# Kernel tuning notes

Hardware: AMD Instinct MI355X
Metric: run time of the kernel (lower is better)

## Reference

```python
import math
import jax, jax.numpy as jnp
import numpy as np
from jax import lax

UP = 2
DOWN = 2
M = 8
BETA = 2.5
FC = 0.5          # up_fc = down_fc = 0.5 (not 'critical' branch)
LRELU = 0.1

def _lpf_filter(factor):
    # Kaiser-windowed sinc, matches Resampler.__init__ (fc != 'critical' branch)
    Mf = M * factor
    n = np.arange(-Mf // 2, Mf // 2 + 1).astype(np.float32)   # 17 taps
    cutoff = FC * math.pi
    f = np.sin(cutoff * n) / (math.pi * n + 1e-8)
    f[len(n) // 2] = FC
    win = np.kaiser(Mf + 1, BETA).astype(np.float32)          # == torch.kaiser_window(.., periodic=False)
    return jnp.asarray(win * f, dtype=jnp.float32)

UP_FILT = _lpf_filter(UP)
DOWN_FILT = _lpf_filter(DOWN)

def _conv1d_same(x, w, groups=1):
    # x: (B, Cin, L), w: (Cout, Cin//groups, K) with odd K
    pad = (w.shape[-1] - 1) // 2
    return lax.conv_general_dilated(x, w, window_strides=(1,), padding=[(pad, pad)],
                                    dimension_numbers=('NCH', 'OIH', 'NCH'),
                                    feature_group_count=groups)

def _lpf(x, filt):
    # depthwise grouped FIR, padding='same'
    C = x.shape[1]
    f = jnp.broadcast_to(filt[None, None, :], (C, 1, filt.shape[0]))
    return _conv1d_same(x, f, groups=C)

def setup_inputs() -> dict:
    key = jax.random.key(0)
    ks = jax.random.split(key, 4)
    bs, c_in, c_out, w_dim, L, k = 16, 512, 512, 512, 2048, 3
    return {
        'x': jax.random.normal(ks[0], (bs, c_in, L), dtype=jnp.float32),
        'w': jax.random.normal(ks[1], (bs, w_dim), dtype=jnp.float32),
        'affine_w': jax.random.normal(ks[2], (c_in, w_dim), dtype=jnp.float32) * 0.02,
        'affine_b': jnp.ones((c_in,), dtype=jnp.float32),
        'conv_w': jax.random.normal(ks[3], (c_out, c_in, k), dtype=jnp.float32) * 0.05,
        'conv_b': jnp.zeros((c_out,), dtype=jnp.float32),
        'norm_ema': jnp.ones((), dtype=jnp.float32),
    }

def reference(x, w, affine_w, affine_b, conv_w, conv_b, norm_ema):
    # eval mode, equalized_lr=False, normalize=True
    x = x * lax.rsqrt(norm_ema)
    cond = w @ affine_w.T + affine_b                                      # (bs, c_in)
    # weight / style normalization
    Wn = conv_w * lax.rsqrt(jnp.mean(jnp.square(conv_w), axis=(1, 2), keepdims=True))
    s = cond * lax.rsqrt(jnp.mean(jnp.square(cond)))                      # (bs, c_in)
    # demod coeff: rsqrt(sum_{i,k} (Wn[o,i,k]*s[b,i])^2 + 1e-8)
    d = lax.rsqrt(jnp.einsum('oik,bi->bo', jnp.square(Wn), jnp.square(s)) + 1e-8)
    # modulate-conv-demodulate (equivalent to per-sample grouped conv with conv_w[None]*s*d)
    y = _conv1d_same(x * s[:, :, None], Wn) * d[:, :, None] + conv_b[None, :, None]
    # upsample: zero-insertion then interpolation LPF
    bs, C, L = y.shape
    y = jnp.pad(y[..., None], ((0, 0), (0, 0), (0, 0), (0, UP - 1))).reshape(bs, C, L * UP)
    y = _lpf(y, UP_FILT)
    # filtered nonlinearity
    y = jax.nn.leaky_relu(y, LRELU) * math.sqrt(2)
    # downsample: anti-alias LPF then decimate
    y = _lpf(y, DOWN_FILT)[:, :, ::DOWN]
    return y
```

## Files before the change

### kernel.cpp

```cpp
#include <hip/hip_runtime.h>
#include <cmath>

typedef __attribute__((ext_vector_type(8))) short short8;
typedef __attribute__((ext_vector_type(4))) float f32x4;

static __device__ __forceinline__ unsigned short f2bf(float x) {
  unsigned int u = __float_as_uint(x);
  unsigned int r = (u + 0x7FFFu + ((u >> 16) & 1u)) >> 16;
  return (unsigned short)r;
}
static __device__ __forceinline__ float bf2f(unsigned short u) {
  return __uint_as_float(((unsigned int)u) << 16);
}
static __device__ __forceinline__ void glds16(const unsigned short* g, unsigned short* l) {
  __builtin_amdgcn_global_load_lds((const __attribute__((address_space(1))) unsigned int*)(g),
                                   (__attribute__((address_space(3))) unsigned int*)(l), 16, 0, 0);
}

#define VWAIT(n) asm volatile("s_waitcnt vmcnt(" #n ")" ::: "memory")

__global__ __launch_bounds__(256) void k_pre1(const float* __restrict__ w,
    const float* __restrict__ aw, const float* __restrict__ ab,
    const float* __restrict__ cw, float* __restrict__ cond, float* __restrict__ ssum,
    float* __restrict__ W2, float* __restrict__ rinv, unsigned short* __restrict__ wpack) {
  __shared__ float red[4];
  int bid = blockIdx.x, t = threadIdx.x;
  if (bid < 128) {
    int outp = bid * 64 + (t >> 2);
    int sub = t & 3;
    int b = outp >> 9, i = outp & 511;
    const float4* wr = (const float4*)(w + b * 512);
    const float4* ar = (const float4*)(aw + i * 512);
    float acc = 0.f;
    #pragma unroll
    for (int jj = 0; jj < 32; ++jj) {
      int j = sub + jj * 4;
      float4 a = ar[j], v = wr[j];
      acc += a.x * v.x + a.y * v.y + a.z * v.z + a.w * v.w;
    }
    acc += __shfl_xor(acc, 1);
    acc += __shfl_xor(acc, 2);
    float s = 0.f;
    if (sub == 0) {
      float c = acc + ab[i];
      cond[outp] = c;
      s = c * c;
    }
    #pragma unroll
    for (int off = 4; off <= 32; off <<= 1) s += __shfl_xor(s, off);
    if ((t & 63) == 0) atomicAdd(ssum, s);
  } else {
    int o = bid - 128;
    const float* row = cw + o * 1536;
    float local = 0.f;
    for (int r = 0; r < 2; ++r) {
      int i = t + 256 * r;
      float a = row[3 * i], b = row[3 * i + 1], c = row[3 * i + 2];
      float w2 = a * a + b * b + c * c;
      W2[o * 512 + i] = w2;
      local += w2;
      int chunk = i >> 5;
      int laneo = (((i >> 3) & 3) << 4) + (o & 15);
      int e = i & 7;
      int base = (chunk * 32 + (o >> 4)) * 512 + laneo * 8 + e;
      wpack[base] = f2bf(a);
      wpack[base + 16 * 32 * 512] = f2bf(b);
      wpack[base + 2 * 16 * 32 * 512] = f2bf(c);
    }
    #pragma unroll
    for (int off = 32; off >= 1; off >>= 1) local += __shfl_down(local, off);
    if ((t & 63) == 0) red[t >> 6] = local;
    __syncthreads();
    if (t == 0) {
      float m = red[0] + red[1] + red[2] + red[3];
      rinv[o] = rsqrtf(m * (1.f / 1536.f));
    }
  }
}

__global__ __launch_bounds__(256) void k_pre2(const float* __restrict__ x,
    const float* __restrict__ W2, const float* __restrict__ cond,
    const float* __restrict__ rinv, const float* __restrict__ ssum,
    const float* __restrict__ nrm, float* __restrict__ coef,
    unsigned short* __restrict__ xsT) {
  __shared__ float shb[64 * 65];
  int bid = blockIdx.x, t = threadIdx.x;
  if (bid < 256) {
    int og = bid & 15, b = bid >> 4;
    int o = og * 32 + (t >> 3);
    int il = t & 7;
    float c0 = cond[b * 512 + t];
    float c1 = cond[b * 512 + t + 256];
    shb[t] = c0 * c0;
    shb[t + 256] = c1 * c1;
    __syncthreads();
    float acc = 0.f;
    #pragma unroll
    for (int jj = 0; jj < 16; ++jj) {
      int i = jj * 32 + il * 4;
      float4 wv = *(const float4*)(W2 + o * 512 + i);
      acc += wv.x * shb[i] + wv.y * shb[i + 1] + wv.z * shb[i + 2] + wv.w * shb[i + 3];
    }
    acc += __shfl_xor(acc, 1);
    acc += __shfl_xor(acc, 2);
    acc += __shfl_xor(acc, 4);
    if (il == 0) {
      float inv_ms = 8192.f / ssum[0];
      float ro = rinv[o];
      coef[b * 512 + o] = ro * rsqrtf(ro * ro * acc * inv_ms + 1e-8f);
    }
  } else {
    int xb = bid - 256;
    int lb = xb & 31, ib = (xb >> 5) & 7, b = xb >> 8;
    float (*tile)[65] = (float(*)[65])shb;
    int l0 = lb * 64, i0 = ib * 64;
    float sc = rsqrtf(ssum[0] * (1.f / 8192.f)) * rsqrtf(nrm[0]);
    int tr = t >> 4, tc = (t & 15) * 4;
    #pragma unroll
    for (int rr = 0; rr < 4; ++rr) {
      int il = rr * 16 + tr;
      float se = cond[b * 512 + i0 + il] * sc;
      float4 v = *(const float4*)(x + ((size_t)b * 512 + i0 + il) * 2048 + l0 + tc);
      tile[il][tc + 0] = v.x * se;
      tile[il][tc + 1] = v.y * se;
      tile[il][tc + 2] = v.z * se;
      tile[il][tc + 3] = v.w * se;
    }
    __syncthreads();
    int lr = t >> 3, ic = (t & 7) * 8;
    #pragma unroll
    for (int rr = 0; rr < 2; ++rr) {
      int ll = rr * 32 + lr;
      uint4 u;
      unsigned int pk[4];
      #pragma unroll
      for (int j = 0; j < 4; ++j) {
        unsigned short lo = f2bf(tile[ic + 2 * j][ll]);
        unsigned short hi = f2bf(tile[ic + 2 * j + 1][ll]);
        pk[j] = (unsigned int)lo | ((unsigned int)hi << 16);
      }
      u.x = pk[0]; u.y = pk[1]; u.z = pk[2]; u.w = pk[3];
      *(uint4*)(xsT + ((size_t)b * 2050 + 1 + l0 + ll) * 512 + i0 + ic) = u;
    }
    if (lb == 0 && t < 8) {
      uint4 z; z.x = 0; z.y = 0; z.z = 0; z.w = 0;
      *(uint4*)(xsT + ((size_t)b * 2050) * 512 + i0 + t * 8) = z;
    }
    if (lb == 31 && t < 8) {
      uint4 z; z.x = 0; z.y = 0; z.z = 0; z.w = 0;
      *(uint4*)(xsT + ((size_t)b * 2050 + 2049) * 512 + i0 + t * 8) = z;
    }
  }
}

#define STAGE_B(buf, c) { \
  _Pragma("unroll") for (int j_ = 0; j_ < 3; ++j_) { \
    int sb_ = wave * 130 + ((j_ < 2) ? j_ * 64 : 128); \
    int s_ = sb_ + ((j_ < 2) ? lane : (lane & 1)); \
    if (j_ < 2 || lane < 2) { \
      int col_ = ((s_ >> 3) << 1) | (((s_ >> 2) ^ (s_ >> 4)) & 1); \
      int q_ = ((s_ ^ (s_ >> 2) ^ (s_ >> 4)) & 1) | ((((s_ >> 1) ^ (s_ >> 3)) & 1) << 1); \
      const unsigned short* src_ = xsT + ((size_t)b * 2050 + l0 + col_) * 512 + (c) * 32 + q_ * 8; \
      glds16(src_, &Bl[buf][sb_ * 8]); \
    } \
  } }

#define LOAD_A(Ar, c) { \
  _Pragma("unroll") for (int k_ = 0; k_ < 3; ++k_) \
  _Pragma("unroll") for (int rg_ = 0; rg_ < 4; ++rg_) \
    Ar[k_ * 4 + rg_] = *(const short8*)(wpack + ((size_t)((k_ * 16 + (c)) * 32 + ob * 8 + wr * 4 + rg_)) * 512 + lane * 8); }

#define MFMA_STEP(Ar, buf) { \
  _Pragma("unroll") for (int k_ = 0; k_ < 3; ++k_) { \
    short8 bfr_[4]; \
    _Pragma("unroll") for (int cg_ = 0; cg_ < 4; ++cg_) { \
      int col_ = wc * 64 + cg_ * 16 + (lane & 15) + k_; \
      int byte_ = (col_ * 64 + ((lane >> 4) << 4)) ^ ((col_ & 7) << 4); \
      bfr_[cg_] = *(const short8*)((const char*)Bl[buf] + byte_); \
    } \
    _Pragma("unroll") for (int rg_ = 0; rg_ < 4; ++rg_) \
      _Pragma("unroll") for (int cg_ = 0; cg_ < 4; ++cg_) \
        acc[rg_][cg_] = __builtin_amdgcn_mfma_f32_16x16x32_bf16(Ar[k_ * 4 + rg_], bfr_[cg_], acc[rg_][cg_], 0, 0, 0); \
  } }

__global__ __launch_bounds__(256, 2) void k_main(const unsigned short* __restrict__ xsT,
    const unsigned short* __restrict__ wpack, const float* __restrict__ coef,
    const float* __restrict__ convb, unsigned short* __restrict__ y) {
  int lb = blockIdx.x, ob = blockIdx.y, b = blockIdx.z;
  int t = threadIdx.x, lane = t & 63, wave = t >> 6;
  int wr = wave >> 1, wc = wave & 1;
  int l0 = lb * 128, o0 = ob * 128;
  __shared__ __align__(16) unsigned short Bl[3][4160];
  f32x4 acc[4][4];
  f32x4 z4 = {0.f, 0.f, 0.f, 0.f};
  #pragma unroll
  for (int i = 0; i < 4; ++i)
    #pragma unroll
    for (int j = 0; j < 4; ++j) acc[i][j] = z4;

  short8 Areg[2][12];
  LOAD_A(Areg[0], 0);
  STAGE_B(0, 0);
  STAGE_B(1, 1);
  __builtin_amdgcn_sched_barrier(0);
  VWAIT(3);
  __builtin_amdgcn_s_barrier();

  #pragma unroll
  for (int c = 0; c < 14; ++c) {
    LOAD_A(Areg[(c + 1) & 1], c + 1);
    STAGE_B((c + 2) % 3, c + 2);
    __builtin_amdgcn_sched_barrier(0);
    MFMA_STEP(Areg[c & 1], c % 3);
    __builtin_amdgcn_sched_barrier(0);
    VWAIT(15);
    __builtin_amdgcn_s_barrier();
  }
  LOAD_A(Areg[1], 15);
  __builtin_amdgcn_sched_barrier(0);
  MFMA_STEP(Areg[0], 2);
  __builtin_amdgcn_sched_barrier(0);
  VWAIT(12);
  __builtin_amdgcn_s_barrier();
  MFMA_STEP(Areg[1], 0);

  int lq = lane >> 4, lrr = lane & 15;
  #pragma unroll
  for (int rg = 0; rg < 4; ++rg) {
    int o2 = o0 + wr * 64 + rg * 16 + lq * 4;
    float c0 = coef[b * 512 + o2 + 0], c1 = coef[b * 512 + o2 + 1];
    float c2 = coef[b * 512 + o2 + 2], c3 = coef[b * 512 + o2 + 3];
    float b0 = convb[o2 + 0], b1 = convb[o2 + 1];
    float b2 = convb[o2 + 2], b3 = convb[o2 + 3];
    #pragma unroll
    for (int cg = 0; cg < 4; ++cg) {
      int l = l0 + wc * 64 + cg * 16 + lrr;
      y[((size_t)b * 512 + o2 + 0) * 4096 + l] = f2bf(acc[rg][cg][0] * c0 + b0);
      y[((size_t)b * 512 + o2 + 1) * 4096 + l] = f2bf(acc[rg][cg][1] * c1 + b1);
      y[((size_t)b * 512 + o2 + 2) * 4096 + l] = f2bf(acc[rg][cg][2] * c2 + b2);
      y[((size_t)b * 512 + o2 + 3) * 4096 + l] = f2bf(acc[rg][cg][3] * c3 + b3);
    }
  }
}

struct Taps { float f[8]; };

__global__ __launch_bounds__(256) void k_filter(const unsigned short* __restrict__ ybuf,
    float* __restrict__ out, Taps tp) {
  int ch = blockIdx.x;
  int t = threadIdx.x;
  __shared__ float ysb[2336];
  const unsigned short* yc = ybuf + (size_t)ch * 4096;
  uint4 v = *(const uint4*)(yc + 8 * t);
  unsigned int wsv[4] = {v.x, v.y, v.z, v.w};
  int phys0 = 9 * t + 9;
  #pragma unroll
  for (int p = 0; p < 4; ++p) {
    ysb[phys0 + 2 * p]     = bf2f((unsigned short)(wsv[p] & 0xffffu));
    ysb[phys0 + 2 * p + 1] = bf2f((unsigned short)(wsv[p] >> 16));
  }
  if (t < 8) ysb[t] = 0.f;
  if (t >= 240 && t < 255) {
    int j = 2056 + (t - 240);
    ysb[j + (j >> 3)] = 0.f;
  }
  __syncthreads();
  float r[22];
  int jb = 8 * t + 1;
  #pragma unroll
  for (int u = 0; u < 22; ++u) { int j = jb + u; r[u] = ysb[j + (j >> 3)]; }
  int m0 = 8 * t;
  float ao[15];
  #pragma unroll
  for (int vv = 0; vv < 15; ++vv) {
    int t4 = m0 - 4 + vv;
    float u = 0.f;
    #pragma unroll
    for (int p = 0; p < 8; ++p) u += tp.f[p] * r[vv + p];
    float a = (u >= 0.f ? u : 0.1f * u) * 1.41421356237309515f;
    ao[vv] = ((unsigned)t4 < 2048u) ? a : 0.f;
  }
  float res[8];
  #pragma unroll
  for (int w = 0; w < 8; ++w) {
    float yv = r[w + 7];
    float s = 0.35355339059327379f * (yv >= 0.f ? yv : 0.1f * yv);
    #pragma unroll
    for (int q = 0; q < 8; ++q) s += tp.f[q] * ao[w + q];
    res[w] = s;
  }
  float4 o0; o0.x = res[0]; o0.y = res[1]; o0.z = res[2]; o0.w = res[3];
  float4 o1; o1.x = res[4]; o1.y = res[5]; o1.z = res[6]; o1.w = res[7];
  float* orow = out + (size_t)ch * 2048 + m0;
  *(float4*)orow = o0;
  *((float4*)orow + 1) = o1;
}

static double bessel_i0(double x) {
  double s = 1.0, term = 1.0;
  for (int m = 1; m < 30; ++m) {
    double h = x * 0.5 / (double)m;
    term *= h * h;
    s += term;
  }
  return s;
}

extern "C" void kernel_launch(void* const* d_in, const int* in_sizes, int n_in,
                              void* d_out, int out_size, void* d_ws, size_t ws_size,
                              hipStream_t stream) {
  (void)in_sizes; (void)n_in; (void)out_size; (void)ws_size;
  const float* x  = (const float*)d_in[0];
  const float* w  = (const float*)d_in[1];
  const float* aw = (const float*)d_in[2];
  const float* ab = (const float*)d_in[3];
  const float* cw = (const float*)d_in[4];
  const float* cb = (const float*)d_in[5];
  const float* ne = (const float*)d_in[6];
  float* out = (float*)d_out;
  char* ws = (char*)d_ws;

  float* ssum = (float*)(ws + 0);
  float* cond = (float*)(ws + 4096);
  float* coef = (float*)(ws + 36864);
  float* rinv = (float*)(ws + 69632);
  unsigned short* wpack = (unsigned short*)(ws + 73728);
  float* W2 = (float*)(ws + 3219456);
  unsigned short* xsT = (unsigned short*)(ws + 4268032);

  hipMemsetAsync(ssum, 0, 4, stream);
  k_pre1<<<640, 256, 0, stream>>>(w, aw, ab, cw, cond, ssum, W2, rinv, wpack);
  k_pre2<<<4352, 256, 0, stream>>>(x, W2, cond, rinv, ssum, ne, coef, xsT);
  k_main<<<dim3(16, 4, 16), 256, 0, stream>>>(xsT, wpack, coef, cb, (unsigned short*)d_out);

  Taps tp;
  {
    double beta = 2.5;
    double i0b = bessel_i0(beta);
    for (int p = 0; p < 8; ++p) {
      int j = 2 * p + 1;
      int n = j - 8;
      double f = sin(0.5 * M_PI * (double)n) / (M_PI * (double)n + 1e-8);
      double rr = (double)(j - 8) / 8.0;
      double win = bessel_i0(beta * sqrt(1.0 - rr * rr)) / i0b;
      tp.f[p] = (float)(win * f);
    }
  }
  k_filter<<<8192, 256, 0, stream>>>((const unsigned short*)d_out, out, tp);
}
```

Baseline: 203.4 us.

## Restructure main GEMM pipeline to paired K-steps and filter to direct global loads

The main MFMA kernel changes from a three-buffer, register-double-buffered A pipeline to a two-parity by two-substep LDS layout. It uses a single A register set reloaded before each MFMA step and a full vmcnt(0) wait with a barrier every two K-chunks. This frees A registers and halves barrier count, but A loads are no longer prefetched ahead of their use, so load latency may be exposed. Separately, the filter kernel drops its LDS staging and syncthreads and instead reads the overlapping bf16 neighbourhood straight from global memory into registers, at the cost of redundant global reads per thread.

```diff
diff --git a/kernel.cpp b/kernel.cpp
--- a/kernel.cpp
+++ b/kernel.cpp
@@ -153,7 +153,7 @@
   }
 }
 
-#define STAGE_B(buf, c) { \
+#define STAGE_B(par, sub, c) { \
   _Pragma("unroll") for (int j_ = 0; j_ < 3; ++j_) { \
     int sb_ = wave * 130 + ((j_ < 2) ? j_ * 64 : 128); \
     int s_ = sb_ + ((j_ < 2) ? lane : (lane & 1)); \
@@ -161,7 +161,7 @@
       int col_ = ((s_ >> 3) << 1) | (((s_ >> 2) ^ (s_ >> 4)) & 1); \
       int q_ = ((s_ ^ (s_ >> 2) ^ (s_ >> 4)) & 1) | ((((s_ >> 1) ^ (s_ >> 3)) & 1) << 1); \
       const unsigned short* src_ = xsT + ((size_t)b * 2050 + l0 + col_) * 512 + (c) * 32 + q_ * 8; \
-      glds16(src_, &Bl[buf][sb_ * 8]); \
+      glds16(src_, &Bl[par][sub][sb_ * 8]); \
     } \
   } }
 
@@ -170,13 +170,13 @@
   _Pragma("unroll") for (int rg_ = 0; rg_ < 4; ++rg_) \
     Ar[k_ * 4 + rg_] = *(const short8*)(wpack + ((size_t)((k_ * 16 + (c)) * 32 + ob * 8 + wr * 4 + rg_)) * 512 + lane * 8); }
 
-#define MFMA_STEP(Ar, buf) { \
+#define MFMA_STEP(Ar, par, sub) { \
   _Pragma("unroll") for (int k_ = 0; k_ < 3; ++k_) { \
     short8 bfr_[4]; \
     _Pragma("unroll") for (int cg_ = 0; cg_ < 4; ++cg_) { \
       int col_ = wc * 64 + cg_ * 16 + (lane & 15) + k_; \
       int byte_ = (col_ * 64 + ((lane >> 4) << 4)) ^ ((col_ & 7) << 4); \
-      bfr_[cg_] = *(const short8*)((const char*)Bl[buf] + byte_); \
+      bfr_[cg_] = *(const short8*)((const char*)Bl[par][sub] + byte_); \
     } \
     _Pragma("unroll") for (int rg_ = 0; rg_ < 4; ++rg_) \
       _Pragma("unroll") for (int cg_ = 0; cg_ < 4; ++cg_) \
@@ -190,7 +190,7 @@
   int t = threadIdx.x, lane = t & 63, wave = t >> 6;
   int wr = wave >> 1, wc = wave & 1;
   int l0 = lb * 128, o0 = ob * 128;
-  __shared__ __align__(16) unsigned short Bl[3][4160];
+  __shared__ __align__(16) unsigned short Bl[2][2][4160];
   f32x4 acc[4][4];
   f32x4 z4 = {0.f, 0.f, 0.f, 0.f};
   #pragma unroll
@@ -198,31 +198,27 @@
     #pragma unroll
     for (int j = 0; j < 4; ++j) acc[i][j] = z4;
 
-  short8 Areg[2][12];
-  LOAD_A(Areg[0], 0);
-  STAGE_B(0, 0);
-  STAGE_B(1, 1);
-  __builtin_amdgcn_sched_barrier(0);
-  VWAIT(3);
+  short8 A[12];
+  STAGE_B(0, 0, 0);
+  STAGE_B(0, 1, 1);
+  VWAIT(0);
   __builtin_amdgcn_s_barrier();
 
   #pragma unroll
-  for (int c = 0; c < 14; ++c) {
-    LOAD_A(Areg[(c + 1) & 1], c + 1);
-    STAGE_B((c + 2) % 3, c + 2);
+  for (int p = 0; p < 8; ++p) {
+    LOAD_A(A, 2 * p);
+    if (p < 7) STAGE_B((p + 1) & 1, 0, 2 * p + 2);
     __builtin_amdgcn_sched_barrier(0);
-    MFMA_STEP(Areg[c & 1], c % 3);
+    MFMA_STEP(A, p & 1, 0);
     __builtin_amdgcn_sched_barrier(0);
-    VWAIT(15);
+    LOAD_A(A, 2 * p + 1);
+    if (p < 7) STAGE_B((p + 1) & 1, 1, 2 * p + 3);
+    __builtin_amdgcn_sched_barrier(0);
+    MFMA_STEP(A, p & 1, 1);
+    __builtin_amdgcn_sched_barrier(0);
+    VWAIT(0);
     __builtin_amdgcn_s_barrier();
   }
-  LOAD_A(Areg[1], 15);
-  __builtin_amdgcn_sched_barrier(0);
-  MFMA_STEP(Areg[0], 2);
-  __builtin_amdgcn_sched_barrier(0);
-  VWAIT(12);
-  __builtin_amdgcn_s_barrier();
-  MFMA_STEP(Areg[1], 0);
 
   int lq = lane >> 4, lrr = lane & 15;
   #pragma unroll
@@ -248,43 +244,48 @@
 __global__ __launch_bounds__(256) void k_filter(const unsigned short* __restrict__ ybuf,
     float* __restrict__ out, Taps tp) {
   int ch = blockIdx.x;
-  int t = threadIdx.x;
-  __shared__ float ysb[2336];
-  const unsigned short* yc = ybuf + (size_t)ch * 4096;
-  uint4 v = *(const uint4*)(yc + 8 * t);
-  unsigned int wsv[4] = {v.x, v.y, v.z, v.w};
-  int phys0 = 9 * t + 9;
-  #pragma unroll
-  for (int p = 0; p < 4; ++p) {
-    ysb[phys0 + 2 * p]     = bf2f((unsigned short)(wsv[p] & 0xffffu));
-    ysb[phys0 + 2 * p + 1] = bf2f((unsigned short)(wsv[p] >> 16));
-  }
-  if (t < 8) ysb[t] = 0.f;
-  if (t >= 240 && t < 255) {
-    int j = 2056 + (t - 240);
-    ysb[j + (j >> 3)] = 0.f;
-  }
-  __syncthreads();
-  float r[22];
-  int jb = 8 * t + 1;
-  #pragma unroll
-  for (int u = 0; u < 22; ++u) { int j = jb + u; r[u] = ysb[j + (j >> 3)]; }
-  int m0 = 8 * t;
+  int tir = threadIdx.x;
+  int m0 = tir * 8;
+  const unsigned short* yr = ybuf + (size_t)ch * 4096;
+  uint4 z; z.x = 0u; z.y = 0u; z.z = 0u; z.w = 0u;
+  uint4 v0, v1, v2;
+  if (tir == 0) {
+    v0 = z;
+    v1 = *(const uint4*)(yr);
+    v2 = *(const uint4*)(yr + 8);
+  } else {
+    const unsigned short* p = yr + m0 - 8;
+    v0 = *(const uint4*)(p);
+    v1 = *(const uint4*)(p + 8);
+    v2 = *(const uint4*)(p + 16);
+    if (tir == 255) v2 = z;
+  }
+  float f[24];
+  {
+    unsigned int wv[12] = {v0.x, v0.y, v0.z, v0.w, v1.x, v1.y, v1.z, v1.w,
+                           v2.x, v2.y, v2.z, v2.w};
+    #pragma unroll
+    for (int s = 0; s < 12; ++s) {
+      f[2 * s]     = bf2f((unsigned short)(wv[s] & 0xffffu));
+      f[2 * s + 1] = bf2f((unsigned short)(wv[s] >> 16));
+    }
+  }
+  const float s2 = 1.41421356237309515f;
   float ao[15];
   #pragma unroll
   for (int vv = 0; vv < 15; ++vv) {
-    int t4 = m0 - 4 + vv;
     float u = 0.f;
     #pragma unroll
-    for (int p = 0; p < 8; ++p) u += tp.f[p] * r[vv + p];
-    float a = (u >= 0.f ? u : 0.1f * u) * 1.41421356237309515f;
-    ao[vv] = ((unsigned)t4 < 2048u) ? a : 0.f;
-  }
+    for (int p = 0; p < 8; ++p) u += tp.f[p] * f[vv + p + 1];
+    float a = (u >= 0.f ? u : 0.1f * u) * s2;
+    ao[vv] = ((unsigned)(m0 - 4 + vv) < 2048u) ? a : 0.f;
+  }
+  const float ce = 0.35355339059327379f;
   float res[8];
   #pragma unroll
   for (int w = 0; w < 8; ++w) {
-    float yv = r[w + 7];
-    float s = 0.35355339059327379f * (yv >= 0.f ? yv : 0.1f * yv);
+    float yv = f[w + 8];
+    float s = ce * (yv >= 0.f ? yv : 0.1f * yv);
     #pragma unroll
     for (int q = 0; q < 8; ++q) s += tp.f[q] * ao[w + q];
     res[w] = s;
```

New measurement: 208.1 us. 1.02x slower.
